# Kernel tuning notes

Hardware: AMD Instinct MI355X
Metric: run time of the kernel (lower is better)

Reference implementation:

```python
import jax, jax.numpy as jnp
import numpy as np

D_MODEL = 4096
NUM_EXPERTS = 64
TOP_K = 8


def setup_inputs() -> dict:
    key = jax.random.key(0)
    kx, kw = jax.random.split(key)
    x = jax.random.normal(kx, (4, 4096, D_MODEL), dtype=jnp.float32)
    # nn.Linear weight [num_experts, d_model]; y = x @ W.T
    W = jax.random.normal(kw, (NUM_EXPERTS, D_MODEL), dtype=jnp.float32) * (1.0 / np.sqrt(D_MODEL))
    return {"x": x, "W": W}


def reference(x, W):
    # logits: [b, s, e]
    logits = jnp.einsum('bsd,ed->bse', x, W)
    router_probs = jax.nn.softmax(logits, axis=-1)
    top_k_weights, top_k_indices = jax.lax.top_k(router_probs, TOP_K)
    top_k_weights = top_k_weights / (jnp.sum(top_k_weights, axis=-1, keepdims=True) + 1e-9)
    return top_k_weights, top_k_indices, router_probs
```

## Files before the change

kernel.cpp:

```cpp
#include <hip/hip_runtime.h>
#include <math.h>

#define D_MODEL 4096
#define NEXP    64
#define TOPK    8
#define NTOK    16384
#define BLK_TOK 64
#define DC      64
#define KSPLIT  4
#define KQ      (D_MODEL / KSPLIT)
#define NCHUNK_Q (KQ / DC)
#define EPW     8
#define NWAVE   (NEXP / EPW)
#define NTHR    (NWAVE * 64)

#define WT2_FLOATS (NEXP * D_MODEL)

__global__ void transpose_w_kernel(const float* __restrict__ W, float* __restrict__ WT2,
                                   float* __restrict__ out_p, int* __restrict__ cnt) {
    int o = blockIdx.x * 256 + threadIdx.x;
    int j = o & 7;
    int d = (o >> 3) & (D_MODEL - 1);
    int g = o >> 15;
    WT2[o] = W[(size_t)(g * 8 + j) * D_MODEL + d];
    *(float4*)&out_p[(size_t)o * 4] = make_float4(0.f, 0.f, 0.f, 0.f);
    if (o == 0) *cnt = 0;
}

__global__ __launch_bounds__(NTHR)
void router_kernel(const float* __restrict__ x, const float* __restrict__ WT2,
                   float* __restrict__ Pacc) {
    __shared__ __align__(16) float lds[2 * 4096];

    const int tid  = threadIdx.x;
    const int lane = tid & 63;
    const int g    = __builtin_amdgcn_readfirstlane(tid >> 6);
    const int s    = blockIdx.x & 3;
    const int tok0 = (blockIdx.x >> 2) * BLK_TOK;
    const int kbase = s * KQ;

    const int row  = tid >> 3;
    const int q    = tid & 7;

    float acc[EPW];
#pragma unroll
    for (int j = 0; j < EPW; ++j) acc[j] = 0.f;

    float4 xr[2];
    const float* xbase = x + (size_t)(tok0 + row) * D_MODEL + kbase + q * 4;
    const float* wk    = WT2 + (g << 15);

    auto load_chunk = [&](int d0) {
#pragma unroll
        for (int j = 0; j < 2; ++j)
            xr[j] = *(const float4*)(xbase + d0 + j * 32);
    };
    auto store_chunk = [&](int buf) {
#pragma unroll
        for (int j = 0; j < 2; ++j)
            *(float4*)&lds[buf * 4096 + (q + j * 8) * 256 + ((row ^ q) << 2)] = xr[j];
    };
    auto compute_chunk = [&](int buf, int kk) {
        const float* wc = wk + (kbase + kk * DC) * 8;
        const float* xb = &lds[buf * 4096];
#pragma unroll 4
        for (int d4 = 0; d4 < DC / 4; ++d4) {
            const float4 xq = *(const float4*)(xb + d4 * 256 + ((lane ^ (d4 & 7)) << 2));
            const float* wd = wc + d4 * 32;
#pragma unroll
            for (int dd = 0; dd < 4; ++dd) {
                const float xv = (dd == 0) ? xq.x : (dd == 1) ? xq.y : (dd == 2) ? xq.z : xq.w;
#pragma unroll
                for (int j = 0; j < 8; ++j)
                    acc[j] = fmaf(xv, wd[dd * 8 + j], acc[j]);
            }
        }
    };

    load_chunk(0);
    store_chunk(0);
    __syncthreads();

    for (int kk = 0; kk < NCHUNK_Q; ++kk) {
        if (kk + 1 < NCHUNK_Q) load_chunk((kk + 1) * DC);
        compute_chunk(kk & 1, kk);
        if (kk + 1 < NCHUNK_Q) store_chunk((kk + 1) & 1);
        __syncthreads();
    }

    float* lg = lds;
#pragma unroll
    for (int j = 0; j < EPW; ++j)
        lg[lane * 65 + g * EPW + j] = acc[j];
    __syncthreads();

    for (int i = tid; i < BLK_TOK * 16; i += NTHR) {
        const int t  = i >> 4;
        const int e4 = (i & 15) << 2;
        const float* src = &lg[t * 65 + e4];
        float* dst = &Pacc[(size_t)(tok0 + t) * NEXP + e4];
#pragma unroll
        for (int c = 0; c < 4; ++c) atomicAdd(dst + c, src[c]);
    }
}

__global__ __launch_bounds__(256)
void finalize_kernel(float* out_p, float* __restrict__ out_w, float* __restrict__ out_i,
                     int* __restrict__ cnt, int* __restrict__ list) {
    __shared__ float lg[BLK_TOK * 65];
    const int tid  = threadIdx.x;
    const int tok0 = blockIdx.x * BLK_TOK;

    for (int i = tid; i < BLK_TOK * 16; i += 256) {
        const int t  = i >> 4;
        const int e4 = (i & 15) << 2;
        const float4 a = *(const float4*)&out_p[(size_t)(tok0 + t) * NEXP + e4];
        float* dst = &lg[t * 65 + e4];
        dst[0] = a.x; dst[1] = a.y; dst[2] = a.z; dst[3] = a.w;
    }
    __syncthreads();

    if (tid < 64) {
        const int tok = tok0 + tid;
        float p[64];
        float m = -INFINITY;
#pragma unroll
        for (int e = 0; e < 64; ++e) {
            p[e] = lg[tid * 65 + e];
            m = fmaxf(m, p[e]);
        }
        float z = 0.f;
#pragma unroll
        for (int e = 0; e < 64; ++e) {
            p[e] = __expf(p[e] - m);
            z += p[e];
        }
        const float rz = 1.f / z;
#pragma unroll
        for (int e = 0; e < 64; ++e) {
            p[e] *= rz;
            lg[tid * 65 + e] = p[e];
        }

        float tv[9]; int ti[9];
#pragma unroll
        for (int k = 0; k < 9; ++k) { tv[k] = -1.f; ti[k] = 0; }
        for (int e = 0; e < 64; ++e) {
            float v = p[e]; int idx = e;
#pragma unroll
            for (int k = 0; k < 9; ++k) {
                const bool gt = v > tv[k];
                const float nv = gt ? v : tv[k];
                const int   ni = gt ? idx : ti[k];
                const float ov = gt ? tv[k] : v;
                const int   oi = gt ? ti[k] : idx;
                tv[k] = nv; ti[k] = ni; v = ov; idx = oi;
            }
        }
        int flag = 0;
#pragma unroll
        for (int k = 0; k < 8; ++k)
            if (tv[k] - tv[k + 1] <= tv[k] * 2e-4f + 1e-12f) flag = 1;
        if (flag) {
            int sidx = atomicAdd(cnt, 1);
            list[sidx] = tok;
        }

        float s8 = 0.f;
#pragma unroll
        for (int k = 0; k < 8; ++k) s8 += tv[k];
        const float denom = s8 + 1e-9f;
#pragma unroll
        for (int k = 0; k < 8; ++k) {
            out_w[tok * TOPK + k] = tv[k] / denom;
            out_i[tok * TOPK + k] = (float)ti[k];
        }
    }
    __syncthreads();

    for (int i = tid; i < BLK_TOK * 16; i += 256) {
        const int t  = i >> 4;
        const int e4 = (i & 15) << 2;
        const float* src = &lg[t * 65 + e4];
        *(float4*)&out_p[(size_t)(tok0 + t) * NEXP + e4] =
            make_float4(src[0], src[1], src[2], src[3]);
    }
}

__global__ __launch_bounds__(256)
void repair_kernel(const float* __restrict__ x, const float* __restrict__ W,
                   const int* __restrict__ cnt, const int* __restrict__ list,
                   float* __restrict__ out_w, float* __restrict__ out_i) {
    __shared__ float  xs[D_MODEL];
    __shared__ double ls[4][NEXP];
    const int tid = threadIdx.x;
    const int e   = tid & 63;
    const int w4  = tid >> 6;
    const int n   = cnt[0];

    for (int i = blockIdx.x; i < n; i += gridDim.x) {
        const int tok = list[i];
        __syncthreads();
        const float4* xsrc = (const float4*)(x + (size_t)tok * D_MODEL);
        for (int v = tid; v < D_MODEL / 4; v += 256)
            ((float4*)xs)[v] = xsrc[v];
        __syncthreads();

        const float* wrow = W + (size_t)e * D_MODEL + w4 * (D_MODEL / 4);
        const float* xrow = xs + w4 * (D_MODEL / 4);
        double s0 = 0., s1 = 0., s2 = 0., s3 = 0.;
        for (int d = 0; d < D_MODEL / 4; d += 4) {
            const float4 wv = *(const float4*)(wrow + d);
            const float4 xv = *(const float4*)(xrow + d);
            s0 += (double)xv.x * (double)wv.x;
            s1 += (double)xv.y * (double)wv.y;
            s2 += (double)xv.z * (double)wv.z;
            s3 += (double)xv.w * (double)wv.w;
        }
        ls[w4][e] = (s0 + s1) + (s2 + s3);
        __syncthreads();

        if (tid == 0) {
            double lsum[64];
            for (int k = 0; k < 64; ++k)
                lsum[k] = (ls[0][k] + ls[1][k]) + (ls[2][k] + ls[3][k]);
            double m = -1e300;
            for (int k = 0; k < 64; ++k) m = lsum[k] > m ? lsum[k] : m;
            double p[64], Z = 0.;
            for (int k = 0; k < 64; ++k) { p[k] = exp(lsum[k] - m); Z += p[k]; }
            for (int k = 0; k < 64; ++k) p[k] /= Z;

            double tv[8]; int ti[8];
            for (int k = 0; k < 8; ++k) { tv[k] = -1.; ti[k] = 0; }
            for (int k = 0; k < 64; ++k) {
                double v = p[k]; int idx = k;
                for (int u = 0; u < 8; ++u) {
                    const bool gt = v > tv[u];
                    const double nv = gt ? v : tv[u];
                    const int    ni = gt ? idx : ti[u];
                    const double ov = gt ? tv[u] : v;
                    const int    oi = gt ? ti[u] : idx;
                    tv[u] = nv; ti[u] = ni; v = ov; idx = oi;
                }
            }
            double s8 = 0.;
            for (int k = 0; k < 8; ++k) s8 += tv[k];
            const double denom = s8 + 1e-9;
            for (int k = 0; k < 8; ++k) {
                out_w[tok * TOPK + k] = (float)(tv[k] / denom);
                out_i[tok * TOPK + k] = (float)ti[k];
            }
        }
    }
}

extern "C" void kernel_launch(void* const* d_in, const int* in_sizes, int n_in,
                              void* d_out, int out_size, void* d_ws, size_t ws_size,
                              hipStream_t stream) {
    const float* x = (const float*)d_in[0];
    const float* W = (const float*)d_in[1];

    float* WT2  = (float*)d_ws;
    int*   cnt  = (int*)((float*)d_ws + WT2_FLOATS);
    int*   list = cnt + 1;

    float* out   = (float*)d_out;
    float* out_w = out;
    float* out_i = out + NTOK * TOPK;
    float* out_p = out + 2 * NTOK * TOPK;

    transpose_w_kernel<<<WT2_FLOATS / 256, 256, 0, stream>>>(W, WT2, out_p, cnt);
    router_kernel<<<(NTOK / BLK_TOK) * KSPLIT, NTHR, 0, stream>>>(x, WT2, out_p);
    finalize_kernel<<<NTOK / BLK_TOK, 256, 0, stream>>>(out_p, out_w, out_i, cnt, list);
    repair_kernel<<<256, 256, 0, stream>>>(x, W, cnt, list, out_w, out_i);
}
```

Before: 555.4 us.

## Compute router logits with split-bf16 MFMA instead of FP32 FMA

Replaces the scalar FP32 FMA router GEMM with bf16 MFMA (16x16x32), splitting x and W each into hi and lo bf16 parts and summing three products to approximate FP32 accuracy. W is pre-split and re-laid out in the transpose kernel, x is converted in registers, and the LDS staging of x is removed. Blocks are remapped across the grid, and the near-tie threshold that sends tokens to the exact repair path is widened to cover the larger rounding error. This trades the FP32 ALU cost for matrix-core throughput, at the risk of more repaired tokens and reduced accuracy margins.

New measurement: 538.7 us. -3.0%, faster.

```diff
diff --git a/kernel.cpp b/kernel.cpp
--- a/kernel.cpp
+++ b/kernel.cpp
@@ -6,95 +6,97 @@
 #define TOPK    8
 #define NTOK    16384
 #define BLK_TOK 64
-#define DC      64
 #define KSPLIT  4
 #define KQ      (D_MODEL / KSPLIT)
-#define NCHUNK_Q (KQ / DC)
-#define EPW     8
-#define NWAVE   (NEXP / EPW)
-#define NTHR    (NWAVE * 64)
-
-#define WT2_FLOATS (NEXP * D_MODEL)
-
-__global__ void transpose_w_kernel(const float* __restrict__ W, float* __restrict__ WT2,
+#define R_GRID  ((NTOK / BLK_TOK) * KSPLIT)
+
+#define W2_USHORTS (NEXP * D_MODEL * 2)
+
+typedef __attribute__((ext_vector_type(8))) short bf16x8;
+typedef __attribute__((ext_vector_type(4))) float f32x4;
+
+__device__ inline unsigned b16rne(float f) {
+    unsigned u = __float_as_uint(f);
+    return (u + 0x7FFFu + ((u >> 16) & 1u)) >> 16;
+}
+
+__global__ void transpose_w_kernel(const float* __restrict__ W, unsigned short* __restrict__ W2,
                                    float* __restrict__ out_p, int* __restrict__ cnt) {
     int o = blockIdx.x * 256 + threadIdx.x;
-    int j = o & 7;
-    int d = (o >> 3) & (D_MODEL - 1);
-    int g = o >> 15;
-    WT2[o] = W[(size_t)(g * 8 + j) * D_MODEL + d];
+    int i  = o & 7;
+    int e  = (o >> 3) & 63;
+    int kb = o >> 9;
+    float w = W[(size_t)e * D_MODEL + kb * 8 + i];
+    unsigned hb = b16rne(w);
+    float hf = __uint_as_float(hb << 16);
+    unsigned lb = b16rne(w - hf);
+    size_t base = ((size_t)(kb * 64 + e) * 2) * 8 + i;
+    W2[base]     = (unsigned short)hb;
+    W2[base + 8] = (unsigned short)lb;
     *(float4*)&out_p[(size_t)o * 4] = make_float4(0.f, 0.f, 0.f, 0.f);
     if (o == 0) *cnt = 0;
 }
 
-__global__ __launch_bounds__(NTHR)
-void router_kernel(const float* __restrict__ x, const float* __restrict__ WT2,
+__global__ __launch_bounds__(256)
+void router_kernel(const float* __restrict__ x, const unsigned short* __restrict__ W2,
                    float* __restrict__ Pacc) {
-    __shared__ __align__(16) float lds[2 * 4096];
+    __shared__ float lg[BLK_TOK * 65];
 
     const int tid  = threadIdx.x;
     const int lane = tid & 63;
-    const int g    = __builtin_amdgcn_readfirstlane(tid >> 6);
-    const int s    = blockIdx.x & 3;
-    const int tok0 = (blockIdx.x >> 2) * BLK_TOK;
+    const int wv   = __builtin_amdgcn_readfirstlane(tid >> 6);
+
+    const int nb   = (blockIdx.x & 7) * (R_GRID / 8) + (blockIdx.x >> 3);
+    const int s    = nb & 3;
+    const int tok0 = (nb >> 2) * BLK_TOK;
     const int kbase = s * KQ;
 
-    const int row  = tid >> 3;
-    const int q    = tid & 7;
-
-    float acc[EPW];
-#pragma unroll
-    for (int j = 0; j < EPW; ++j) acc[j] = 0.f;
-
-    float4 xr[2];
-    const float* xbase = x + (size_t)(tok0 + row) * D_MODEL + kbase + q * 4;
-    const float* wk    = WT2 + (g << 15);
-
-    auto load_chunk = [&](int d0) {
-#pragma unroll
-        for (int j = 0; j < 2; ++j)
-            xr[j] = *(const float4*)(xbase + d0 + j * 32);
-    };
-    auto store_chunk = [&](int buf) {
-#pragma unroll
-        for (int j = 0; j < 2; ++j)
-            *(float4*)&lds[buf * 4096 + (q + j * 8) * 256 + ((row ^ q) << 2)] = xr[j];
-    };
-    auto compute_chunk = [&](int buf, int kk) {
-        const float* wc = wk + (kbase + kk * DC) * 8;
-        const float* xb = &lds[buf * 4096];
-#pragma unroll 4
-        for (int d4 = 0; d4 < DC / 4; ++d4) {
-            const float4 xq = *(const float4*)(xb + d4 * 256 + ((lane ^ (d4 & 7)) << 2));
-            const float* wd = wc + d4 * 32;
-#pragma unroll
-            for (int dd = 0; dd < 4; ++dd) {
-                const float xv = (dd == 0) ? xq.x : (dd == 1) ? xq.y : (dd == 2) ? xq.z : xq.w;
-#pragma unroll
-                for (int j = 0; j < 8; ++j)
-                    acc[j] = fmaf(xv, wd[dd * 8 + j], acc[j]);
-            }
-        }
-    };
-
-    load_chunk(0);
-    store_chunk(0);
+    const int l15 = lane & 15;
+    const int kg  = lane >> 4;
+
+    f32x4 acc[4];
+#pragma unroll
+    for (int nt = 0; nt < 4; ++nt) acc[nt] = (f32x4)0.f;
+
+    const float* xrow = x + (size_t)(tok0 + wv * 16 + l15) * D_MODEL + kbase + kg * 8;
+    const unsigned short* wbase = W2 + ((size_t)(((kbase >> 3) + kg) * 64 + l15) * 2) * 8;
+
+    for (int ks = 0; ks < KQ / 32; ++ks) {
+        const float4 xa = *(const float4*)(xrow + ks * 32);
+        const float4 xb = *(const float4*)(xrow + ks * 32 + 4);
+
+        union { unsigned u[4]; bf16x8 v; } Ahi, Alo;
+#pragma unroll
+        for (int p = 0; p < 4; ++p) {
+            const float f0 = (p == 0) ? xa.x : (p == 1) ? xa.z : (p == 2) ? xb.x : xb.z;
+            const float f1 = (p == 0) ? xa.y : (p == 1) ? xa.w : (p == 2) ? xb.y : xb.w;
+            const unsigned h0 = b16rne(f0), h1 = b16rne(f1);
+            Ahi.u[p] = h0 | (h1 << 16);
+            const float l0 = f0 - __uint_as_float(h0 << 16);
+            const float l1 = f1 - __uint_as_float(h1 << 16);
+            Alo.u[p] = b16rne(l0) | (b16rne(l1) << 16);
+        }
+
+        const unsigned short* wk = wbase + (size_t)ks * 4096;
+#pragma unroll
+        for (int nt = 0; nt < 4; ++nt) {
+            const unsigned short* wp = wk + nt * 256;
+            const bf16x8 bhi = *(const bf16x8*)(wp);
+            const bf16x8 blo = *(const bf16x8*)(wp + 8);
+            acc[nt] = __builtin_amdgcn_mfma_f32_16x16x32_bf16(Ahi.v, bhi, acc[nt], 0, 0, 0);
+            acc[nt] = __builtin_amdgcn_mfma_f32_16x16x32_bf16(Ahi.v, blo, acc[nt], 0, 0, 0);
+            acc[nt] = __builtin_amdgcn_mfma_f32_16x16x32_bf16(Alo.v, bhi, acc[nt], 0, 0, 0);
+        }
+    }
+
+#pragma unroll
+    for (int nt = 0; nt < 4; ++nt)
+#pragma unroll
+        for (int r = 0; r < 4; ++r)
+            lg[(wv * 16 + kg * 4 + r) * 65 + nt * 16 + l15] = acc[nt][r];
     __syncthreads();
 
-    for (int kk = 0; kk < NCHUNK_Q; ++kk) {
-        if (kk + 1 < NCHUNK_Q) load_chunk((kk + 1) * DC);
-        compute_chunk(kk & 1, kk);
-        if (kk + 1 < NCHUNK_Q) store_chunk((kk + 1) & 1);
-        __syncthreads();
-    }
-
-    float* lg = lds;
-#pragma unroll
-    for (int j = 0; j < EPW; ++j)
-        lg[lane * 65 + g * EPW + j] = acc[j];
-    __syncthreads();
-
-    for (int i = tid; i < BLK_TOK * 16; i += NTHR) {
+    for (int i = tid; i < BLK_TOK * 16; i += 256) {
         const int t  = i >> 4;
         const int e4 = (i & 15) << 2;
         const float* src = &lg[t * 65 + e4];
@@ -160,7 +162,7 @@
         int flag = 0;
 #pragma unroll
         for (int k = 0; k < 8; ++k)
-            if (tv[k] - tv[k + 1] <= tv[k] * 2e-4f + 1e-12f) flag = 1;
+            if (tv[k] - tv[k + 1] <= tv[k] * 4e-4f + 1e-9f) flag = 1;
         if (flag) {
             int sidx = atomicAdd(cnt, 1);
             list[sidx] = tok;
@@ -260,17 +262,17 @@
     const float* x = (const float*)d_in[0];
     const float* W = (const float*)d_in[1];
 
-    float* WT2  = (float*)d_ws;
-    int*   cnt  = (int*)((float*)d_ws + WT2_FLOATS);
-    int*   list = cnt + 1;
+    unsigned short* W2 = (unsigned short*)d_ws;
+    int* cnt  = (int*)(W2 + W2_USHORTS);
+    int* list = cnt + 1;
 
     float* out   = (float*)d_out;
     float* out_w = out;
     float* out_i = out + NTOK * TOPK;
     float* out_p = out + 2 * NTOK * TOPK;
 
-    transpose_w_kernel<<<WT2_FLOATS / 256, 256, 0, stream>>>(W, WT2, out_p, cnt);
-    router_kernel<<<(NTOK / BLK_TOK) * KSPLIT, NTHR, 0, stream>>>(x, WT2, out_p);
+    transpose_w_kernel<<<262144 / 256, 256, 0, stream>>>(W, W2, out_p, cnt);
+    router_kernel<<<R_GRID, 256, 0, stream>>>(x, W2, out_p);
     finalize_kernel<<<NTOK / BLK_TOK, 256, 0, stream>>>(out_p, out_w, out_i, cnt, list);
     repair_kernel<<<256, 256, 0, stream>>>(x, W, cnt, list, out_w, out_i);
 }
```
